# Performance work log

Hardware: AMD Instinct MI355X
Metric: run time of the kernel (lower is better)

The kernel has to match this reference:

```python
import jax, jax.numpy as jnp
import numpy as np

N, E = 50000, 800000
IN_D, HID_D, OUT_D = 128, 64, 64
EPS_BN = 1e-5
NEG_SLOPE = 0.2


def _xavier(key, shape):
    fan_in, fan_out = shape[0], shape[-1]
    lim = float(np.sqrt(6.0 / (fan_in + fan_out)))
    return jax.random.uniform(key, shape, jnp.float32, -lim, lim)


def setup_inputs() -> dict:
    key = jax.random.key(0)
    ks = jax.random.split(key, 10)
    x = jax.random.normal(ks[0], (N, IN_D), jnp.float32)
    edge_index = jax.random.randint(ks[1], (2, E), 0, N, jnp.int64)
    return {
        "x": x,
        "edge_index": edge_index,
        "W1": _xavier(ks[2], (IN_D, HID_D)),
        "att_src1": _xavier(ks[3], (1, HID_D))[0],
        "att_dst1": _xavier(ks[4], (1, HID_D))[0],
        "bias1": jnp.zeros((HID_D,), jnp.float32),
        "gamma": jnp.ones((HID_D,), jnp.float32),
        "beta": jnp.zeros((HID_D,), jnp.float32),
        "W2": _xavier(ks[5], (HID_D, OUT_D)),
        "att_src2": _xavier(ks[6], (1, OUT_D))[0],
        "att_dst2": _xavier(ks[7], (1, OUT_D))[0],
        "bias2": jnp.zeros((OUT_D,), jnp.float32),
    }


def _gat_conv(x, src, dst, W, a_src, a_dst, bias, n_nodes):
    # h: [N, D_out]; messages flow src -> dst; softmax over edges per dst node
    h = x @ W
    alpha_s = h @ a_src  # [N]
    alpha_d = h @ a_dst  # [N]
    e = jax.nn.leaky_relu(alpha_s[src] + alpha_d[dst], NEG_SLOPE)  # [E]
    e_max = jax.ops.segment_max(e, dst, num_segments=n_nodes)
    e = jnp.exp(e - e_max[dst])
    denom = jax.ops.segment_sum(e, dst, num_segments=n_nodes)
    alpha = e / (denom[dst] + 1e-16)  # [E]
    out = jax.ops.segment_sum(h[src] * alpha[:, None], dst, num_segments=n_nodes)
    return out + bias


def _batchnorm(x, gamma, beta):
    mu = jnp.mean(x, axis=0)
    var = jnp.var(x, axis=0)
    return (x - mu) * jax.lax.rsqrt(var + EPS_BN) * gamma + beta


def reference(x, edge_index, W1, att_src1, att_dst1, bias1, gamma, beta,
              W2, att_src2, att_dst2, bias2):
    n_nodes = x.shape[0]
    loops = jnp.arange(n_nodes, dtype=edge_index.dtype)
    src = jnp.concatenate([edge_index[0], loops])  # add self loops (PyG default)
    dst = jnp.concatenate([edge_index[1], loops])
    h = _gat_conv(x, src, dst, W1, att_src1, att_dst1, bias1, n_nodes)
    h = jax.nn.relu(_batchnorm(h, gamma, beta))
    return _gat_conv(h, src, dst, W2, att_src2, att_dst2, bias2, n_nodes)
```

## Files before the change

kernel.cpp:

```cpp
#include <hip/hip_runtime.h>

#define N_NODES 50000
#define E_EDGES 800000
#define NE_TOT  (E_EDGES + N_NODES)
#define IND     128
#define HID     64
#define CAP_X   32
#define NEG_SLOPE 0.2f
#define GEMM_BLKS ((N_NODES + 63) / 64)
#define EDGE_BLKS ((NE_TOT + 255) / 256)

typedef short v8s __attribute__((ext_vector_type(8)));
typedef float v4f __attribute__((ext_vector_type(4)));

#define SWZ(row, byte) ((byte) ^ (((row) & 7) << 4))

static __device__ __forceinline__ unsigned short f2bf(float f) {
    unsigned u = __float_as_uint(f);
    return (unsigned short)((u + 0x7FFF + ((u >> 16) & 1)) >> 16);
}
static __device__ __forceinline__ float bf2f(unsigned short u) {
    return __uint_as_float(((unsigned)u) << 16);
}

__global__ void k_init(const float* __restrict__ W1, const float* __restrict__ W2,
                       int* __restrict__ cnt, float* __restrict__ sums,
                       unsigned short* __restrict__ w1t, unsigned short* __restrict__ w2t) {
    int g = blockIdx.x * 256 + threadIdx.x;
    if (g < 8 * N_NODES) cnt[g] = 0;
    if (g < 128) sums[g] = 0.f;
    if (g < 64 * IND) { int c = g >> 7, k = g & 127; w1t[g] = f2bf(W1[k * 64 + c]); }
    if (g < 64 * 64)  { int c = g >> 6, k = g & 63;  w2t[g] = f2bf(W2[k * 64 + c]); }
}

__global__ __launch_bounds__(256) void k_fused1(
    const float* __restrict__ x, const unsigned short* __restrict__ w1t,
    const float* __restrict__ as_w, const float* __restrict__ ad_w,
    unsigned short* __restrict__ hbf, float* __restrict__ as_out, float* __restrict__ ad_out,
    const int* __restrict__ ei, int* __restrict__ cnt, unsigned short* __restrict__ bucket)
{
    __shared__ __align__(16) char sA[64 * 256];
    __shared__ __align__(16) char sB[64 * 256];
    __shared__ float sAs[64], sAd[64];
    int tid = threadIdx.x;

    if (blockIdx.x >= GEMM_BLKS) {
        int xcc;
        asm("s_getreg_b32 %0, hwreg(20, 0, 32)" : "=s"(xcc));
        xcc &= 7;
        int e = (blockIdx.x - GEMM_BLKS) * 256 + tid;
        if (e >= NE_TOT) return;
        int s, d;
        if (e < E_EDGES) { s = ei[e]; d = ei[E_EDGES + e]; }
        else { s = d = e - E_EDGES; }
        int pos = atomicAdd(&cnt[xcc * N_NODES + d], 1);
        if (pos < CAP_X) bucket[((size_t)(xcc * CAP_X + pos)) * N_NODES + d] = (unsigned short)s;
        return;
    }

    int row0 = blockIdx.x * 64;
#pragma unroll
    for (int i = 0; i < 8; ++i) {
        int idx = i * 256 + tid;
        int r = idx >> 5, c4 = idx & 31;
        int gr = row0 + r; if (gr >= N_NODES) gr = N_NODES - 1;
        float4 v = ((const float4*)(x + (size_t)gr * IND))[c4];
        ushort4 b; b.x = f2bf(v.x); b.y = f2bf(v.y); b.z = f2bf(v.z); b.w = f2bf(v.w);
        *(ushort4*)(sA + r * 256 + SWZ(r, c4 * 8)) = b;
    }
#pragma unroll
    for (int i = 0; i < 4; ++i) {
        int idx = i * 256 + tid;
        int r = idx >> 4, c8 = idx & 15;
        v8s wv = *(const v8s*)(w1t + idx * 8);
        *(v8s*)(sB + r * 256 + SWZ(r, c8 * 16)) = wv;
    }
    if (tid < 64) { sAs[tid] = as_w[tid]; sAd[tid] = ad_w[tid]; }
    __syncthreads();

    int w = tid >> 6, lane = tid & 63;
    int arow = w * 16 + (lane & 15);
    int kb   = (lane >> 4) * 16;
    v4f acc[4] = {};
#pragma unroll
    for (int ks = 0; ks < 4; ++ks) {
        v8s a = *(const v8s*)(sA + arow * 256 + SWZ(arow, ks * 64 + kb));
#pragma unroll
        for (int ct = 0; ct < 4; ++ct) {
            int brow = ct * 16 + (lane & 15);
            v8s b = *(const v8s*)(sB + brow * 256 + SWZ(brow, ks * 64 + kb));
            acc[ct] = __builtin_amdgcn_mfma_f32_16x16x32_bf16(a, b, acc[ct], 0, 0, 0);
        }
    }

    int cbase = lane & 15;
    int rloc  = (lane >> 4) * 4;
#pragma unroll
    for (int ct = 0; ct < 4; ++ct)
#pragma unroll
        for (int rg = 0; rg < 4; ++rg) {
            int row = row0 + w * 16 + rloc + rg;
            if (row < N_NODES) hbf[(size_t)row * 64 + ct * 16 + cbase] = f2bf(acc[ct][rg]);
        }
#pragma unroll
    for (int rg = 0; rg < 4; ++rg) {
        float vs = 0.f, vd = 0.f;
#pragma unroll
        for (int ct = 0; ct < 4; ++ct) {
            vs = fmaf(acc[ct][rg], sAs[ct * 16 + cbase], vs);
            vd = fmaf(acc[ct][rg], sAd[ct * 16 + cbase], vd);
        }
        vs += __shfl_xor(vs, 1, 64); vd += __shfl_xor(vd, 1, 64);
        vs += __shfl_xor(vs, 2, 64); vd += __shfl_xor(vd, 2, 64);
        vs += __shfl_xor(vs, 4, 64); vd += __shfl_xor(vd, 4, 64);
        vs += __shfl_xor(vs, 8, 64); vd += __shfl_xor(vd, 8, 64);
        int row = row0 + w * 16 + rloc + rg;
        if (cbase == 0 && row < N_NODES) { as_out[row] = vs; ad_out[row] = vd; }
    }
}

template <bool OUT_BF16>
__global__ __launch_bounds__(256) void k_agg(
    const unsigned short* __restrict__ hin, const float* __restrict__ as_, const float* __restrict__ ad_,
    const int* __restrict__ cnt, const unsigned short* __restrict__ bucket,
    const float* __restrict__ bias, void* __restrict__ outv)
{
    int wave = threadIdx.x >> 6, lane = threadIdx.x & 63;
    int n = blockIdx.x * 4 + wave;
    if (n >= N_NODES) return;

    int pref[9]; pref[0] = 0;
#pragma unroll
    for (int xx = 0; xx < 8; ++xx)
        pref[xx + 1] = pref[xx] + min(cnt[xx * N_NODES + n], CAP_X);
    int deg = min(pref[8], 64);

    int xseg = 0, base = 0;
#pragma unroll
    for (int i = 0; i < 7; ++i)
        if (lane >= pref[i + 1]) { xseg = i + 1; base = pref[i + 1]; }

    float adn = ad_[n];
    int s_l = 0;
    float e = -1e30f;
    if (lane < deg) {
        s_l = (int)bucket[((size_t)(xseg * CAP_X + (lane - base))) * N_NODES + n];
        float t = as_[s_l] + adn;
        e = t > 0.f ? t : NEG_SLOPE * t;
    }
    float m = e;
    for (int off = 32; off; off >>= 1) m = fmaxf(m, __shfl_xor(m, off, 64));
    float w_l = (lane < deg) ? __expf(e - m) : 0.f;
    float denom = w_l;
    for (int off = 32; off; off >>= 1) denom += __shfl_xor(denom, off, 64);

    int g = lane >> 4, fb = (lane & 15) * 4;
    float a0 = 0.f, a1 = 0.f, a2 = 0.f, a3 = 0.f;
    for (int t = 0; t < deg; t += 8) {
        int sa = __shfl(s_l, t + g);
        int sb = __shfl(s_l, t + 4 + g);
        float wa = __shfl(w_l, t + g);
        float wb = __shfl(w_l, t + 4 + g);
        ushort4 ha = {0, 0, 0, 0}, hb = {0, 0, 0, 0};
        if (t + g < deg)     ha = *(const ushort4*)(hin + (size_t)sa * HID + fb);
        if (t + 4 + g < deg) hb = *(const ushort4*)(hin + (size_t)sb * HID + fb);
        a0 = fmaf(wa, bf2f(ha.x), a0); a1 = fmaf(wa, bf2f(ha.y), a1);
        a2 = fmaf(wa, bf2f(ha.z), a2); a3 = fmaf(wa, bf2f(ha.w), a3);
        a0 = fmaf(wb, bf2f(hb.x), a0); a1 = fmaf(wb, bf2f(hb.y), a1);
        a2 = fmaf(wb, bf2f(hb.z), a2); a3 = fmaf(wb, bf2f(hb.w), a3);
    }
    a0 += __shfl_xor(a0, 16, 64); a0 += __shfl_xor(a0, 32, 64);
    a1 += __shfl_xor(a1, 16, 64); a1 += __shfl_xor(a1, 32, 64);
    a2 += __shfl_xor(a2, 16, 64); a2 += __shfl_xor(a2, 32, 64);
    a3 += __shfl_xor(a3, 16, 64); a3 += __shfl_xor(a3, 32, 64);

    if (lane < 16) {
        float inv = 1.f / (denom + 1e-16f);
        float4 b4 = ((const float4*)bias)[lane];
        float r0 = fmaf(a0, inv, b4.x), r1 = fmaf(a1, inv, b4.y);
        float r2 = fmaf(a2, inv, b4.z), r3 = fmaf(a3, inv, b4.w);
        if (OUT_BF16) {
            ushort4 o; o.x = f2bf(r0); o.y = f2bf(r1); o.z = f2bf(r2); o.w = f2bf(r3);
            *(ushort4*)((unsigned short*)outv + (size_t)n * HID + lane * 4) = o;
        } else {
            float4 o = {r0, r1, r2, r3};
            *(float4*)((float*)outv + (size_t)n * HID + lane * 4) = o;
        }
    }
}

__global__ __launch_bounds__(256) void k_bnstats(const unsigned short* __restrict__ h,
                                                 float* __restrict__ sums) {
    int lane = threadIdx.x & 63, wave = threadIdx.x >> 6;
    float s = 0.f, ss = 0.f;
    for (int r = blockIdx.x * 4 + wave; r < N_NODES; r += gridDim.x * 4) {
        float v = bf2f(h[(size_t)r * HID + lane]);
        s += v; ss = fmaf(v, v, ss);
    }
    __shared__ float ls[4][64], lss[4][64];
    ls[wave][lane] = s; lss[wave][lane] = ss;
    __syncthreads();
    if (wave == 0) {
        s  = ls[0][lane] + ls[1][lane] + ls[2][lane] + ls[3][lane];
        ss = lss[0][lane] + lss[1][lane] + lss[2][lane] + lss[3][lane];
        atomicAdd(&sums[lane], s);
        atomicAdd(&sums[64 + lane], ss);
    }
}

__global__ __launch_bounds__(256) void k_gemm2(
    const unsigned short* __restrict__ hin, const unsigned short* __restrict__ w2t,
    const float* __restrict__ sums, const float* __restrict__ gamma, const float* __restrict__ beta,
    const float* __restrict__ as_w, const float* __restrict__ ad_w,
    unsigned short* __restrict__ h2bf, float* __restrict__ as_out, float* __restrict__ ad_out)
{
    __shared__ __align__(16) char sA[64 * 128];
    __shared__ __align__(16) char sB[64 * 128];
    __shared__ float sAs[64], sAd[64], sScale[64], sShift[64];
    int tid = threadIdx.x;
    int row0 = blockIdx.x * 64;

    if (tid < 64) {
        float mean = sums[tid] * (1.f / N_NODES);
        float var  = sums[64 + tid] * (1.f / N_NODES) - mean * mean;
        float sc = gamma[tid] * rsqrtf(var + 1e-5f);
        sScale[tid] = sc;
        sShift[tid] = beta[tid] - mean * sc;
        sAs[tid] = as_w[tid]; sAd[tid] = ad_w[tid];
    }
    __syncthreads();

#pragma unroll
    for (int i = 0; i < 2; ++i) {
        int idx = i * 256 + tid;
        int r = idx >> 3, c8 = idx & 7;
        int gr = row0 + r; if (gr >= N_NODES) gr = N_NODES - 1;
        v8s hv = *(const v8s*)(hin + (size_t)gr * 64 + c8 * 8);
        unsigned short o[8];
#pragma unroll
        for (int j = 0; j < 8; ++j) {
            float f = bf2f((unsigned short)hv[j]);
            o[j] = f2bf(fmaxf(fmaf(f, sScale[c8 * 8 + j], sShift[c8 * 8 + j]), 0.f));
        }
        *(v8s*)(sA + r * 128 + SWZ(r, c8 * 16)) = *(v8s*)o;
    }
#pragma unroll
    for (int i = 0; i < 2; ++i) {
        int idx = i * 256 + tid;
        int r = idx >> 3, c8 = idx & 7;
        v8s wv = *(const v8s*)(w2t + idx * 8);
        *(v8s*)(sB + r * 128 + SWZ(r, c8 * 16)) = wv;
    }
    __syncthreads();

    int w = tid >> 6, lane = tid & 63;
    int arow = w * 16 + (lane & 15);
    int kb   = (lane >> 4) * 16;
    v4f acc[4] = {};
#pragma unroll
    for (int ks = 0; ks < 2; ++ks) {
        v8s a = *(const v8s*)(sA + arow * 128 + SWZ(arow, ks * 64 + kb));
#pragma unroll
        for (int ct = 0; ct < 4; ++ct) {
            int brow = ct * 16 + (lane & 15);
            v8s b = *(const v8s*)(sB + brow * 128 + SWZ(brow, ks * 64 + kb));
            acc[ct] = __builtin_amdgcn_mfma_f32_16x16x32_bf16(a, b, acc[ct], 0, 0, 0);
        }
    }

    int cbase = lane & 15;
    int rloc  = (lane >> 4) * 4;
#pragma unroll
    for (int ct = 0; ct < 4; ++ct)
#pragma unroll
        for (int rg = 0; rg < 4; ++rg) {
            int row = row0 + w * 16 + rloc + rg;
            if (row < N_NODES) h2bf[(size_t)row * 64 + ct * 16 + cbase] = f2bf(acc[ct][rg]);
        }
#pragma unroll
    for (int rg = 0; rg < 4; ++rg) {
        float vs = 0.f, vd = 0.f;
#pragma unroll
        for (int ct = 0; ct < 4; ++ct) {
            vs = fmaf(acc[ct][rg], sAs[ct * 16 + cbase], vs);
            vd = fmaf(acc[ct][rg], sAd[ct * 16 + cbase], vd);
        }
        vs += __shfl_xor(vs, 1, 64); vd += __shfl_xor(vd, 1, 64);
        vs += __shfl_xor(vs, 2, 64); vd += __shfl_xor(vd, 2, 64);
        vs += __shfl_xor(vs, 4, 64); vd += __shfl_xor(vd, 4, 64);
        vs += __shfl_xor(vs, 8, 64); vd += __shfl_xor(vd, 8, 64);
        int row = row0 + w * 16 + rloc + rg;
        if (cbase == 0 && row < N_NODES) { as_out[row] = vs; ad_out[row] = vd; }
    }
}

extern "C" void kernel_launch(void* const* d_in, const int* in_sizes, int n_in,
                              void* d_out, int out_size, void* d_ws, size_t ws_size,
                              hipStream_t stream) {
    const float* x        = (const float*)d_in[0];
    const int*   ei       = (const int*)d_in[1];
    const float* W1       = (const float*)d_in[2];
    const float* att_src1 = (const float*)d_in[3];
    const float* att_dst1 = (const float*)d_in[4];
    const float* bias1    = (const float*)d_in[5];
    const float* gamma    = (const float*)d_in[6];
    const float* beta     = (const float*)d_in[7];
    const float* W2       = (const float*)d_in[8];
    const float* att_src2 = (const float*)d_in[9];
    const float* att_dst2 = (const float*)d_in[10];
    const float* bias2    = (const float*)d_in[11];
    float* out = (float*)d_out;

    char* ws = (char*)d_ws;
    size_t off = 0;
    auto alloc = [&](size_t bytes) { void* p = ws + off; off = (off + bytes + 255) & ~(size_t)255; return p; };
    unsigned short* h1     = (unsigned short*)alloc((size_t)N_NODES * HID * 2);
    float* as1    = (float*)alloc((size_t)N_NODES * 4);
    float* ad1    = (float*)alloc((size_t)N_NODES * 4);
    unsigned short* h1agg  = (unsigned short*)alloc((size_t)N_NODES * HID * 2);
    unsigned short* h2     = (unsigned short*)alloc((size_t)N_NODES * HID * 2);
    float* as2    = (float*)alloc((size_t)N_NODES * 4);
    float* ad2    = (float*)alloc((size_t)N_NODES * 4);
    int*   cnt    = (int*)alloc((size_t)8 * N_NODES * 4);
    unsigned short* bucket = (unsigned short*)alloc((size_t)8 * CAP_X * N_NODES * 2);
    float* sums   = (float*)alloc(128 * 4);
    unsigned short* w1t = (unsigned short*)alloc(64 * IND * 2);
    unsigned short* w2t = (unsigned short*)alloc(64 * 64 * 2);

    int initBlocks = (8 * N_NODES + 255) / 256;
    k_init<<<initBlocks, 256, 0, stream>>>(W1, W2, cnt, sums, w1t, w2t);
    k_fused1<<<GEMM_BLKS + EDGE_BLKS, 256, 0, stream>>>(x, w1t, att_src1, att_dst1,
                                                        h1, as1, ad1, ei, cnt, bucket);
    k_agg<true><<<(N_NODES + 3) / 4, 256, 0, stream>>>(h1, as1, ad1, cnt, bucket, bias1, h1agg);
    k_bnstats<<<256, 256, 0, stream>>>(h1agg, sums);
    k_gemm2<<<GEMM_BLKS, 256, 0, stream>>>(h1agg, w2t, sums, gamma, beta,
                                           att_src2, att_dst2, h2, as2, ad2);
    k_agg<false><<<(N_NODES + 3) / 4, 256, 0, stream>>>(h2, as2, ad2, cnt, bucket, bias2, out);
}
```

Measured before the change: 137.4 us.

## Process two nodes per wave in aggregation and stage GEMM output through LDS

The aggregation kernel now handles two destination nodes per wavefront and interleaves their gather loops, so more independent loads are in flight to hide gather latency. The per-edge bounds checks are dropped by relying on zero weights and index 0 for padding lanes, which adds some wasted loads when the two degrees differ. Both GEMM kernels now write bf16 results into shared memory first and then store them with coalesced 16-byte writes instead of scattered 2-byte stores. The grid size assumes N is divisible by 8.

```diff
diff --git a/kernel.cpp b/kernel.cpp
--- a/kernel.cpp
+++ b/kernel.cpp
@@ -96,13 +96,6 @@
     int cbase = lane & 15;
     int rloc  = (lane >> 4) * 4;
 #pragma unroll
-    for (int ct = 0; ct < 4; ++ct)
-#pragma unroll
-        for (int rg = 0; rg < 4; ++rg) {
-            int row = row0 + w * 16 + rloc + rg;
-            if (row < N_NODES) hbf[(size_t)row * 64 + ct * 16 + cbase] = f2bf(acc[ct][rg]);
-        }
-#pragma unroll
     for (int rg = 0; rg < 4; ++rg) {
         float vs = 0.f, vd = 0.f;
 #pragma unroll
@@ -116,6 +109,21 @@
         vs += __shfl_xor(vs, 8, 64); vd += __shfl_xor(vd, 8, 64);
         int row = row0 + w * 16 + rloc + rg;
         if (cbase == 0 && row < N_NODES) { as_out[row] = vs; ad_out[row] = vd; }
+    }
+    __syncthreads();
+    unsigned short* sC = (unsigned short*)sA;
+#pragma unroll
+    for (int ct = 0; ct < 4; ++ct)
+#pragma unroll
+        for (int rg = 0; rg < 4; ++rg)
+            sC[(w * 16 + rloc + rg) * 64 + ct * 16 + cbase] = f2bf(acc[ct][rg]);
+    __syncthreads();
+    int validc = min(64, N_NODES - row0) * 8;
+#pragma unroll
+    for (int i = 0; i < 2; ++i) {
+        int c = i * 256 + tid;
+        if (c < validc)
+            *(v8s*)(hbf + (size_t)row0 * 64 + c * 8) = *(const v8s*)(sC + c * 8);
     }
 }
 
@@ -126,65 +134,89 @@
     const float* __restrict__ bias, void* __restrict__ outv)
 {
     int wave = threadIdx.x >> 6, lane = threadIdx.x & 63;
-    int n = blockIdx.x * 4 + wave;
-    if (n >= N_NODES) return;
-
-    int pref[9]; pref[0] = 0;
-#pragma unroll
-    for (int xx = 0; xx < 8; ++xx)
-        pref[xx + 1] = pref[xx] + min(cnt[xx * N_NODES + n], CAP_X);
-    int deg = min(pref[8], 64);
-
-    int xseg = 0, base = 0;
-#pragma unroll
-    for (int i = 0; i < 7; ++i)
-        if (lane >= pref[i + 1]) { xseg = i + 1; base = pref[i + 1]; }
-
-    float adn = ad_[n];
-    int s_l = 0;
-    float e = -1e30f;
-    if (lane < deg) {
-        s_l = (int)bucket[((size_t)(xseg * CAP_X + (lane - base))) * N_NODES + n];
-        float t = as_[s_l] + adn;
-        e = t > 0.f ? t : NEG_SLOPE * t;
-    }
-    float m = e;
-    for (int off = 32; off; off >>= 1) m = fmaxf(m, __shfl_xor(m, off, 64));
-    float w_l = (lane < deg) ? __expf(e - m) : 0.f;
-    float denom = w_l;
-    for (int off = 32; off; off >>= 1) denom += __shfl_xor(denom, off, 64);
+    int n0 = blockIdx.x * 8 + wave * 2;
+
+    int deg[2], xseg[2], base[2], s_l[2];
+    float e_[2], m_[2], w_l[2], denom[2];
+
+#pragma unroll
+    for (int j = 0; j < 2; ++j) {
+        int n = n0 + j;
+        int p[9]; p[0] = 0;
+#pragma unroll
+        for (int xx = 0; xx < 8; ++xx)
+            p[xx + 1] = p[xx] + min(cnt[xx * N_NODES + n], CAP_X);
+        deg[j] = min(p[8], 64);
+        int xs = 0, bs = 0;
+#pragma unroll
+        for (int i = 0; i < 7; ++i)
+            if (lane >= p[i + 1]) { xs = i + 1; bs = p[i + 1]; }
+        xseg[j] = xs; base[j] = bs;
+    }
+#pragma unroll
+    for (int j = 0; j < 2; ++j) {
+        s_l[j] = 0; e_[j] = -1e30f;
+        if (lane < deg[j]) {
+            s_l[j] = (int)bucket[((size_t)(xseg[j] * CAP_X + (lane - base[j]))) * N_NODES + n0 + j];
+            float t = as_[s_l[j]] + ad_[n0 + j];
+            e_[j] = t > 0.f ? t : NEG_SLOPE * t;
+        }
+        m_[j] = e_[j];
+    }
+    for (int off = 32; off; off >>= 1) {
+        m_[0] = fmaxf(m_[0], __shfl_xor(m_[0], off, 64));
+        m_[1] = fmaxf(m_[1], __shfl_xor(m_[1], off, 64));
+    }
+#pragma unroll
+    for (int j = 0; j < 2; ++j) {
+        w_l[j] = (lane < deg[j]) ? __expf(e_[j] - m_[j]) : 0.f;
+        denom[j] = w_l[j];
+    }
+    for (int off = 32; off; off >>= 1) {
+        denom[0] += __shfl_xor(denom[0], off, 64);
+        denom[1] += __shfl_xor(denom[1], off, 64);
+    }
 
     int g = lane >> 4, fb = (lane & 15) * 4;
-    float a0 = 0.f, a1 = 0.f, a2 = 0.f, a3 = 0.f;
-    for (int t = 0; t < deg; t += 8) {
-        int sa = __shfl(s_l, t + g);
-        int sb = __shfl(s_l, t + 4 + g);
-        float wa = __shfl(w_l, t + g);
-        float wb = __shfl(w_l, t + 4 + g);
-        ushort4 ha = {0, 0, 0, 0}, hb = {0, 0, 0, 0};
-        if (t + g < deg)     ha = *(const ushort4*)(hin + (size_t)sa * HID + fb);
-        if (t + 4 + g < deg) hb = *(const ushort4*)(hin + (size_t)sb * HID + fb);
-        a0 = fmaf(wa, bf2f(ha.x), a0); a1 = fmaf(wa, bf2f(ha.y), a1);
-        a2 = fmaf(wa, bf2f(ha.z), a2); a3 = fmaf(wa, bf2f(ha.w), a3);
-        a0 = fmaf(wb, bf2f(hb.x), a0); a1 = fmaf(wb, bf2f(hb.y), a1);
-        a2 = fmaf(wb, bf2f(hb.z), a2); a3 = fmaf(wb, bf2f(hb.w), a3);
-    }
-    a0 += __shfl_xor(a0, 16, 64); a0 += __shfl_xor(a0, 32, 64);
-    a1 += __shfl_xor(a1, 16, 64); a1 += __shfl_xor(a1, 32, 64);
-    a2 += __shfl_xor(a2, 16, 64); a2 += __shfl_xor(a2, 32, 64);
-    a3 += __shfl_xor(a3, 16, 64); a3 += __shfl_xor(a3, 32, 64);
+    float a[2][4] = {};
+    int dmax = max(deg[0], deg[1]);
+    for (int t = 0; t < dmax; t += 8) {
+#pragma unroll
+        for (int j = 0; j < 2; ++j) {
+            int sa = __shfl(s_l[j], t + g);
+            int sb = __shfl(s_l[j], t + 4 + g);
+            float wa = __shfl(w_l[j], t + g);
+            float wb = __shfl(w_l[j], t + 4 + g);
+            ushort4 ha = *(const ushort4*)(hin + (size_t)sa * HID + fb);
+            ushort4 hb = *(const ushort4*)(hin + (size_t)sb * HID + fb);
+            a[j][0] = fmaf(wa, bf2f(ha.x), a[j][0]); a[j][1] = fmaf(wa, bf2f(ha.y), a[j][1]);
+            a[j][2] = fmaf(wa, bf2f(ha.z), a[j][2]); a[j][3] = fmaf(wa, bf2f(ha.w), a[j][3]);
+            a[j][0] = fmaf(wb, bf2f(hb.x), a[j][0]); a[j][1] = fmaf(wb, bf2f(hb.y), a[j][1]);
+            a[j][2] = fmaf(wb, bf2f(hb.z), a[j][2]); a[j][3] = fmaf(wb, bf2f(hb.w), a[j][3]);
+        }
+    }
+#pragma unroll
+    for (int j = 0; j < 2; ++j)
+#pragma unroll
+        for (int k = 0; k < 4; ++k) {
+            a[j][k] += __shfl_xor(a[j][k], 16, 64);
+            a[j][k] += __shfl_xor(a[j][k], 32, 64);
+        }
 
     if (lane < 16) {
-        float inv = 1.f / (denom + 1e-16f);
         float4 b4 = ((const float4*)bias)[lane];
-        float r0 = fmaf(a0, inv, b4.x), r1 = fmaf(a1, inv, b4.y);
-        float r2 = fmaf(a2, inv, b4.z), r3 = fmaf(a3, inv, b4.w);
-        if (OUT_BF16) {
-            ushort4 o; o.x = f2bf(r0); o.y = f2bf(r1); o.z = f2bf(r2); o.w = f2bf(r3);
-            *(ushort4*)((unsigned short*)outv + (size_t)n * HID + lane * 4) = o;
-        } else {
-            float4 o = {r0, r1, r2, r3};
-            *(float4*)((float*)outv + (size_t)n * HID + lane * 4) = o;
+#pragma unroll
+        for (int j = 0; j < 2; ++j) {
+            float inv = 1.f / (denom[j] + 1e-16f);
+            float r0 = fmaf(a[j][0], inv, b4.x), r1 = fmaf(a[j][1], inv, b4.y);
+            float r2 = fmaf(a[j][2], inv, b4.z), r3 = fmaf(a[j][3], inv, b4.w);
+            if (OUT_BF16) {
+                ushort4 o; o.x = f2bf(r0); o.y = f2bf(r1); o.z = f2bf(r2); o.w = f2bf(r3);
+                *(ushort4*)((unsigned short*)outv + (size_t)(n0 + j) * HID + lane * 4) = o;
+            } else {
+                float4 o = {r0, r1, r2, r3};
+                *(float4*)((float*)outv + (size_t)(n0 + j) * HID + lane * 4) = o;
+            }
         }
     }
 }
@@ -271,13 +303,6 @@
     int cbase = lane & 15;
     int rloc  = (lane >> 4) * 4;
 #pragma unroll
-    for (int ct = 0; ct < 4; ++ct)
-#pragma unroll
-        for (int rg = 0; rg < 4; ++rg) {
-            int row = row0 + w * 16 + rloc + rg;
-            if (row < N_NODES) h2bf[(size_t)row * 64 + ct * 16 + cbase] = f2bf(acc[ct][rg]);
-        }
-#pragma unroll
     for (int rg = 0; rg < 4; ++rg) {
         float vs = 0.f, vd = 0.f;
 #pragma unroll
@@ -291,6 +316,21 @@
         vs += __shfl_xor(vs, 8, 64); vd += __shfl_xor(vd, 8, 64);
         int row = row0 + w * 16 + rloc + rg;
         if (cbase == 0 && row < N_NODES) { as_out[row] = vs; ad_out[row] = vd; }
+    }
+    __syncthreads();
+    unsigned short* sC = (unsigned short*)sA;
+#pragma unroll
+    for (int ct = 0; ct < 4; ++ct)
+#pragma unroll
+        for (int rg = 0; rg < 4; ++rg)
+            sC[(w * 16 + rloc + rg) * 64 + ct * 16 + cbase] = f2bf(acc[ct][rg]);
+    __syncthreads();
+    int validc = min(64, N_NODES - row0) * 8;
+#pragma unroll
+    for (int i = 0; i < 2; ++i) {
+        int c = i * 256 + tid;
+        if (c < validc)
+            *(v8s*)(h2bf + (size_t)row0 * 64 + c * 8) = *(const v8s*)(sC + c * 8);
     }
 }
 
@@ -331,9 +371,9 @@
     k_init<<<initBlocks, 256, 0, stream>>>(W1, W2, cnt, sums, w1t, w2t);
     k_fused1<<<GEMM_BLKS + EDGE_BLKS, 256, 0, stream>>>(x, w1t, att_src1, att_dst1,
                                                         h1, as1, ad1, ei, cnt, bucket);
-    k_agg<true><<<(N_NODES + 3) / 4, 256, 0, stream>>>(h1, as1, ad1, cnt, bucket, bias1, h1agg);
+    k_agg<true><<<N_NODES / 8, 256, 0, stream>>>(h1, as1, ad1, cnt, bucket, bias1, h1agg);
     k_bnstats<<<256, 256, 0, stream>>>(h1agg, sums);
     k_gemm2<<<GEMM_BLKS, 256, 0, stream>>>(h1agg, w2t, sums, gamma, beta,
                                            att_src2, att_dst2, h2, as2, ad2);
-    k_agg<false><<<(N_NODES + 3) / 4, 256, 0, stream>>>(h2, as2, ad2, cnt, bucket, bias2, out);
-}
+    k_agg<false><<<N_NODES / 8, 256, 0, stream>>>(h2, as2, ad2, cnt, bucket, bias2, out);
+}
```

After: 122.9 us. 10.6% less time.
